# Performance work log

Measured on AMD Instinct MI355X. Metric: run time of the kernel, lower is better.

The kernel has to match this reference:

```python
import jax, jax.numpy as jnp
import numpy as np

LOG2 = float(np.log(2.0))

def ssp(x):
    # shifted softplus: softplus(x) - log(2)
    return jax.nn.softplus(x) - LOG2

N_NODES = 50000
N_EDGES = 600000
HID = 128
NF = 128

def setup_inputs() -> dict:
    key = jax.random.key(0)
    ks = jax.random.split(key, 10)
    x = jax.random.normal(ks[0], (N_NODES, HID), dtype=jnp.float32)
    edge_attr = jax.random.normal(ks[1], (N_EDGES, NF), dtype=jnp.float32)
    edge_index = jax.random.randint(ks[2], (2, N_EDGES), 0, N_NODES, dtype=jnp.int32)
    s = 1.0 / np.sqrt(NF)
    fc1_w = jax.random.uniform(ks[3], (NF, HID), jnp.float32, -s, s)   # CFConv.fc1 (no bias)
    f_w1 = jax.random.uniform(ks[4], (NF, NF), jnp.float32, -s, s)     # filter_mlp[0]
    f_b1 = jnp.zeros((NF,), jnp.float32)
    f_w2 = jax.random.uniform(ks[5], (NF, NF), jnp.float32, -s, s)     # filter_mlp[2]
    f_b2 = jnp.zeros((NF,), jnp.float32)
    s_w1 = jax.random.uniform(ks[6], (NF, NF), jnp.float32, -s, s)     # StateMLP.fc1
    s_w2 = jax.random.uniform(ks[7], (NF, NF), jnp.float32, -s, s)     # StateMLP.fc2
    return {"x": x, "edge_attr": edge_attr, "edge_index": edge_index,
            "fc1_w": fc1_w, "f_w1": f_w1, "f_b1": f_b1, "f_w2": f_w2,
            "f_b2": f_b2, "s_w1": s_w1, "s_w2": s_w2}

def reference(x, edge_attr, edge_index, fc1_w, f_w1, f_b1, f_w2, f_b2, s_w1, s_w2):
    src, dst = edge_index[0], edge_index[1]  # x_j = x[src], aggregate at dst
    # filter network on edge attributes: [E, NF]
    W = ssp(ssp(edge_attr @ f_w1.T + f_b1) @ f_w2.T + f_b2)
    # message: gather source nodes, linear transform, filter multiply
    msg = (x[src] @ fc1_w.T) * W                               # [E, NF]
    # scatter-add aggregation into nodes
    agg = jax.ops.segment_sum(msg, dst, num_segments=x.shape[0])  # [N, NF]
    # StateMLP
    return ssp(agg @ s_w1.T) @ s_w2.T
```

## Files before the change

kernel.cpp:

```cpp
#include <hip/hip_runtime.h>

#define F 128

typedef __attribute__((ext_vector_type(8))) __bf16 bf16x8;
typedef __attribute__((ext_vector_type(4))) float floatx4;

__device__ __forceinline__ float ssp(float x) {
    return __logf(fmaf(0.5f, __expf(x), 0.5f));
}

__global__ void prep_kernel(const float* __restrict__ fc1w,
                            const float* __restrict__ fw1,
                            const float* __restrict__ fw2,
                            const float* __restrict__ sw1,
                            const float* __restrict__ sw2,
                            __bf16* __restrict__ fc1h, __bf16* __restrict__ fc1l,
                            __bf16* __restrict__ fw1h, __bf16* __restrict__ fw2h,
                            __bf16* __restrict__ sw1h, __bf16* __restrict__ sw1l,
                            __bf16* __restrict__ sw2h, __bf16* __restrict__ sw2l)
{
    int i = blockIdx.x * blockDim.x + threadIdx.x;
    if (i >= F * F) return;
    float v; __bf16 h;
    v = fc1w[i]; h = (__bf16)v; fc1h[i] = h; fc1l[i] = (__bf16)(v - (float)h);
    v = sw1[i];  h = (__bf16)v; sw1h[i] = h; sw1l[i] = (__bf16)(v - (float)h);
    v = sw2[i];  h = (__bf16)v; sw2h[i] = h; sw2l[i] = (__bf16)(v - (float)h);
    fw1h[i] = (__bf16)fw1[i];
    fw2h[i] = (__bf16)fw2[i];
}

__global__ __launch_bounds__(256) void fc1_kernel(
    const float* __restrict__ x, const __bf16* __restrict__ wh,
    const __bf16* __restrict__ wl, float* __restrict__ y, int M)
{
    const int tid = threadIdx.x;
    const int wv = tid >> 6, lane = tid & 63;
    const int m16 = lane & 15, q = lane >> 4;
    const int g = wv & 1, c = wv >> 1;
    const int rowA0 = blockIdx.x * 32 + g * 16 + m16;
    const int rowA = rowA0 < M ? rowA0 : M - 1;

    floatx4 acc[4] = {};
    #pragma unroll
    for (int ks = 0; ks < 4; ++ks) {
        const int kb = ks * 32 + q * 8;
        const float4* p = (const float4*)(x + (size_t)rowA * F + kb);
        float4 a0 = p[0], a1 = p[1];
        float fv[8] = {a0.x, a0.y, a0.z, a0.w, a1.x, a1.y, a1.z, a1.w};
        bf16x8 ah, al;
        #pragma unroll
        for (int i = 0; i < 8; ++i) {
            __bf16 h = (__bf16)fv[i];
            ah[i] = h; al[i] = (__bf16)(fv[i] - (float)h);
        }
        #pragma unroll
        for (int nt = 0; nt < 4; ++nt) {
            const size_t wo = (size_t)(c * 64 + nt * 16 + m16) * F + kb;
            bf16x8 bh = *(const bf16x8*)(wh + wo);
            bf16x8 bl = *(const bf16x8*)(wl + wo);
            acc[nt] = __builtin_amdgcn_mfma_f32_16x16x32_bf16(ah, bh, acc[nt], 0, 0, 0);
            acc[nt] = __builtin_amdgcn_mfma_f32_16x16x32_bf16(al, bh, acc[nt], 0, 0, 0);
            acc[nt] = __builtin_amdgcn_mfma_f32_16x16x32_bf16(ah, bl, acc[nt], 0, 0, 0);
        }
    }
    const int rowD0 = blockIdx.x * 32 + g * 16 + q * 4;
    #pragma unroll
    for (int nt = 0; nt < 4; ++nt) {
        const int col = c * 64 + nt * 16 + m16;
        #pragma unroll
        for (int r = 0; r < 4; ++r) {
            const int row = rowD0 + r;
            if (row < M) y[(size_t)row * F + col] = acc[nt][r];
        }
    }
}

__global__ __launch_bounds__(256) void edge_kernel(
    const float* __restrict__ edge_attr,
    const int* __restrict__ eidx,
    const float* __restrict__ fb1, const float* __restrict__ fb2,
    const __bf16* __restrict__ fw1, const __bf16* __restrict__ fw2,
    const float* __restrict__ y,
    float* __restrict__ agg, int E)
{
    __shared__ __bf16 h1[64][136];

    const int tid = threadIdx.x;
    const int wv = tid >> 6, lane = tid & 63;
    const int m16 = lane & 15, q = lane >> 4;
    const int e0 = blockIdx.x * 64;
    const int rowA0 = e0 + wv * 16 + m16;
    const int rowA = rowA0 < E ? rowA0 : E - 1;

    floatx4 acc[8] = {};
    #pragma unroll
    for (int ks = 0; ks < 4; ++ks) {
        const int kb = ks * 32 + q * 8;
        const float4* pa = (const float4*)(edge_attr + (size_t)rowA * F + kb);
        float4 a0 = pa[0], a1 = pa[1];
        float fv[8] = {a0.x, a0.y, a0.z, a0.w, a1.x, a1.y, a1.z, a1.w};
        bf16x8 aF;
        #pragma unroll
        for (int i = 0; i < 8; ++i) aF[i] = (__bf16)fv[i];
        #pragma unroll
        for (int nt = 0; nt < 8; ++nt) {
            bf16x8 bF = *(const bf16x8*)(fw1 + (size_t)(nt * 16 + m16) * F + kb);
            acc[nt] = __builtin_amdgcn_mfma_f32_16x16x32_bf16(aF, bF, acc[nt], 0, 0, 0);
        }
    }
    #pragma unroll
    for (int nt = 0; nt < 8; ++nt) {
        const int col = nt * 16 + m16;
        const float b = fb1[col];
        #pragma unroll
        for (int r = 0; r < 4; ++r) {
            const int row = wv * 16 + q * 4 + r;
            h1[row][col] = (__bf16)ssp(acc[nt][r] + b);
        }
    }
    __syncthreads();

    floatx4 zero = {};
    #pragma unroll
    for (int nt = 0; nt < 8; ++nt) acc[nt] = zero;
    #pragma unroll
    for (int ks = 0; ks < 4; ++ks) {
        const int kb = ks * 32 + q * 8;
        bf16x8 aF = *(const bf16x8*)(&h1[wv * 16 + m16][kb]);
        #pragma unroll
        for (int nt = 0; nt < 8; ++nt) {
            bf16x8 bF = *(const bf16x8*)(fw2 + (size_t)(nt * 16 + m16) * F + kb);
            acc[nt] = __builtin_amdgcn_mfma_f32_16x16x32_bf16(aF, bF, acc[nt], 0, 0, 0);
        }
    }

    int src[4], dst[4], ok[4];
    #pragma unroll
    for (int r = 0; r < 4; ++r) {
        const int e = e0 + wv * 16 + q * 4 + r;
        const int ec = e < E ? e : E - 1;
        ok[r] = (e < E);
        src[r] = eidx[ec];
        dst[r] = eidx[E + ec];
    }
    #pragma unroll
    for (int nt = 0; nt < 8; ++nt) {
        const int col = nt * 16 + m16;
        const float b = fb2[col];
        #pragma unroll
        for (int r = 0; r < 4; ++r) {
            if (ok[r]) {
                const float wV = ssp(acc[nt][r] + b);
                const float v = y[(size_t)src[r] * F + col] * wV;
                unsafeAtomicAdd(&agg[(size_t)dst[r] * F + col], v);
            }
        }
    }
}

__global__ __launch_bounds__(256) void state_kernel(
    const float* __restrict__ agg,
    const __bf16* __restrict__ w1h, const __bf16* __restrict__ w1l,
    const __bf16* __restrict__ w2h, const __bf16* __restrict__ w2l,
    float* __restrict__ out, int M)
{
    __shared__ __bf16 hh[32][136];
    __shared__ __bf16 hl[32][136];

    const int tid = threadIdx.x;
    const int wv = tid >> 6, lane = tid & 63;
    const int m16 = lane & 15, q = lane >> 4;
    const int g = wv & 1, c = wv >> 1;
    const int rowA0 = blockIdx.x * 32 + g * 16 + m16;
    const int rowA = rowA0 < M ? rowA0 : M - 1;

    floatx4 acc[4] = {};
    #pragma unroll
    for (int ks = 0; ks < 4; ++ks) {
        const int kb = ks * 32 + q * 8;
        const float4* p = (const float4*)(agg + (size_t)rowA * F + kb);
        float4 a0 = p[0], a1 = p[1];
        float fv[8] = {a0.x, a0.y, a0.z, a0.w, a1.x, a1.y, a1.z, a1.w};
        bf16x8 ah, al;
        #pragma unroll
        for (int i = 0; i < 8; ++i) {
            __bf16 h = (__bf16)fv[i];
            ah[i] = h; al[i] = (__bf16)(fv[i] - (float)h);
        }
        #pragma unroll
        for (int nt = 0; nt < 4; ++nt) {
            const size_t wo = (size_t)(c * 64 + nt * 16 + m16) * F + kb;
            bf16x8 bh = *(const bf16x8*)(w1h + wo);
            bf16x8 bl = *(const bf16x8*)(w1l + wo);
            acc[nt] = __builtin_amdgcn_mfma_f32_16x16x32_bf16(ah, bh, acc[nt], 0, 0, 0);
            acc[nt] = __builtin_amdgcn_mfma_f32_16x16x32_bf16(al, bh, acc[nt], 0, 0, 0);
            acc[nt] = __builtin_amdgcn_mfma_f32_16x16x32_bf16(ah, bl, acc[nt], 0, 0, 0);
        }
    }
    #pragma unroll
    for (int nt = 0; nt < 4; ++nt) {
        const int col = c * 64 + nt * 16 + m16;
        #pragma unroll
        for (int r = 0; r < 4; ++r) {
            const int row = g * 16 + q * 4 + r;
            const float h = ssp(acc[nt][r]);
            const __bf16 H = (__bf16)h;
            hh[row][col] = H;
            hl[row][col] = (__bf16)(h - (float)H);
        }
    }
    __syncthreads();

    floatx4 zero = {};
    #pragma unroll
    for (int nt = 0; nt < 4; ++nt) acc[nt] = zero;
    #pragma unroll
    for (int ks = 0; ks < 4; ++ks) {
        const int kb = ks * 32 + q * 8;
        bf16x8 aH = *(const bf16x8*)(&hh[g * 16 + m16][kb]);
        bf16x8 aL = *(const bf16x8*)(&hl[g * 16 + m16][kb]);
        #pragma unroll
        for (int nt = 0; nt < 4; ++nt) {
            const size_t wo = (size_t)(c * 64 + nt * 16 + m16) * F + kb;
            bf16x8 bh = *(const bf16x8*)(w2h + wo);
            bf16x8 bl = *(const bf16x8*)(w2l + wo);
            acc[nt] = __builtin_amdgcn_mfma_f32_16x16x32_bf16(aH, bh, acc[nt], 0, 0, 0);
            acc[nt] = __builtin_amdgcn_mfma_f32_16x16x32_bf16(aL, bh, acc[nt], 0, 0, 0);
            acc[nt] = __builtin_amdgcn_mfma_f32_16x16x32_bf16(aH, bl, acc[nt], 0, 0, 0);
        }
    }
    const int rowD0 = blockIdx.x * 32 + g * 16 + q * 4;
    #pragma unroll
    for (int nt = 0; nt < 4; ++nt) {
        const int col = c * 64 + nt * 16 + m16;
        #pragma unroll
        for (int r = 0; r < 4; ++r) {
            const int row = rowD0 + r;
            if (row < M) out[(size_t)row * F + col] = acc[nt][r];
        }
    }
}

extern "C" void kernel_launch(void* const* d_in, const int* in_sizes, int n_in,
                              void* d_out, int out_size, void* d_ws, size_t ws_size,
                              hipStream_t stream)
{
    const float* x         = (const float*)d_in[0];
    const float* edge_attr = (const float*)d_in[1];
    const int*   eidx      = (const int*)d_in[2];
    const float* fc1w      = (const float*)d_in[3];
    const float* fw1       = (const float*)d_in[4];
    const float* fb1       = (const float*)d_in[5];
    const float* fw2       = (const float*)d_in[6];
    const float* fb2       = (const float*)d_in[7];
    const float* sw1       = (const float*)d_in[8];
    const float* sw2       = (const float*)d_in[9];
    float* out = (float*)d_out;

    const int N = in_sizes[0] / F;
    const int E = in_sizes[1] / F;

    float* agg = (float*)d_ws;
    float* y   = agg + (size_t)N * F;
    __bf16* wb = (__bf16*)(y + (size_t)N * F);
    const int WSZ = F * F;
    __bf16* fc1h = wb;            __bf16* fc1l = wb + WSZ;
    __bf16* fw1h = wb + 2 * WSZ;  __bf16* fw2h = wb + 3 * WSZ;
    __bf16* sw1h = wb + 4 * WSZ;  __bf16* sw1l = wb + 5 * WSZ;
    __bf16* sw2h = wb + 6 * WSZ;  __bf16* sw2l = wb + 7 * WSZ;

    hipMemsetAsync(agg, 0, (size_t)N * F * sizeof(float), stream);

    prep_kernel<<<(WSZ + 255) / 256, 256, 0, stream>>>(
        fc1w, fw1, fw2, sw1, sw2, fc1h, fc1l, fw1h, fw2h, sw1h, sw1l, sw2h, sw2l);

    fc1_kernel<<<(N + 31) / 32, 256, 0, stream>>>(x, fc1h, fc1l, y, N);

    edge_kernel<<<(E + 63) / 64, 256, 0, stream>>>(
        edge_attr, eidx, fb1, fb2, fw1h, fw2h, y, agg, E);

    state_kernel<<<(N + 31) / 32, 256, 0, stream>>>(
        agg, sw1h, sw1l, sw2h, sw2l, out, N);
}
```

Before: 931.1 us.

## Sort edges by destination and segment-reduce messages before atomic adds

Builds a counting-sort permutation of edges by destination node (histogram, single-block scan, scatter) and processes edges in that order. Messages are staged in shared memory and each thread reduces runs of equal destination along a column before issuing one atomic add per run. This is meant to cut global atomic traffic sharply, at the cost of extra sort kernels, gathered edge_attr reads and an extra barrier. The bounds guard for a partial last block is dropped.

```diff
diff --git a/kernel.cpp b/kernel.cpp
--- a/kernel.cpp
+++ b/kernel.cpp
@@ -29,6 +29,49 @@
     fw2h[i] = (__bf16)fw2[i];
 }
 
+__global__ void hist_kernel(const int* __restrict__ eidx, int* __restrict__ deg, int E)
+{
+    int e = blockIdx.x * blockDim.x + threadIdx.x;
+    if (e < E) atomicAdd(&deg[eidx[E + e]], 1);
+}
+
+__global__ __launch_bounds__(1024) void scan_kernel(int* __restrict__ cur, int N)
+{
+    __shared__ int part[1024];
+    const int t = threadIdx.x;
+    const int chunk = (N + 1023) / 1024;
+    const int lo = t * chunk;
+    const int hi = (lo + chunk < N) ? lo + chunk : N;
+    int s = 0;
+    for (int i = lo; i < hi; ++i) s += cur[i];
+    part[t] = s;
+    __syncthreads();
+    for (int off = 1; off < 1024; off <<= 1) {
+        int v = part[t];
+        int u = (t >= off) ? part[t - off] : 0;
+        __syncthreads();
+        part[t] = v + u;
+        __syncthreads();
+    }
+    int pre = (t == 0) ? 0 : part[t - 1];
+    for (int i = lo; i < hi; ++i) {
+        int d = cur[i];
+        cur[i] = pre;
+        pre += d;
+    }
+}
+
+__global__ void scatter_kernel(const int* __restrict__ eidx, int* __restrict__ cur,
+                               int* __restrict__ perm, int E)
+{
+    int e = blockIdx.x * blockDim.x + threadIdx.x;
+    if (e < E) {
+        int d = eidx[E + e];
+        int pos = atomicAdd(&cur[d], 1);
+        perm[pos] = e;
+    }
+}
+
 __global__ __launch_bounds__(256) void fc1_kernel(
     const float* __restrict__ x, const __bf16* __restrict__ wh,
     const __bf16* __restrict__ wl, float* __restrict__ y, int M)
@@ -78,25 +121,35 @@
 __global__ __launch_bounds__(256) void edge_kernel(
     const float* __restrict__ edge_attr,
     const int* __restrict__ eidx,
+    const int* __restrict__ perm,
     const float* __restrict__ fb1, const float* __restrict__ fb2,
     const __bf16* __restrict__ fw1, const __bf16* __restrict__ fw2,
     const float* __restrict__ y,
     float* __restrict__ agg, int E)
 {
-    __shared__ __bf16 h1[64][136];
+    __shared__ float msgF[64][132];
+    __shared__ int sOE[64], sSRC[64], sDST[64];
+    __bf16 (*h1)[136] = (__bf16 (*)[136])&msgF[0][0];
 
     const int tid = threadIdx.x;
     const int wv = tid >> 6, lane = tid & 63;
     const int m16 = lane & 15, q = lane >> 4;
     const int e0 = blockIdx.x * 64;
-    const int rowA0 = e0 + wv * 16 + m16;
-    const int rowA = rowA0 < E ? rowA0 : E - 1;
-
+
+    if (tid < 64) {
+        const int oe = perm[e0 + tid];
+        sOE[tid] = oe;
+        sSRC[tid] = eidx[oe];
+        sDST[tid] = eidx[E + oe];
+    }
+    __syncthreads();
+
+    const int aRow = sOE[wv * 16 + m16];
     floatx4 acc[8] = {};
     #pragma unroll
     for (int ks = 0; ks < 4; ++ks) {
         const int kb = ks * 32 + q * 8;
-        const float4* pa = (const float4*)(edge_attr + (size_t)rowA * F + kb);
+        const float4* pa = (const float4*)(edge_attr + (size_t)aRow * F + kb);
         float4 a0 = pa[0], a1 = pa[1];
         float fv[8] = {a0.x, a0.y, a0.z, a0.w, a1.x, a1.y, a1.z, a1.w};
         bf16x8 aF;
@@ -133,29 +186,41 @@
             acc[nt] = __builtin_amdgcn_mfma_f32_16x16x32_bf16(aF, bF, acc[nt], 0, 0, 0);
         }
     }
-
-    int src[4], dst[4], ok[4];
-    #pragma unroll
-    for (int r = 0; r < 4; ++r) {
-        const int e = e0 + wv * 16 + q * 4 + r;
-        const int ec = e < E ? e : E - 1;
-        ok[r] = (e < E);
-        src[r] = eidx[ec];
-        dst[r] = eidx[E + ec];
-    }
+    __syncthreads();
+
+    int srcR[4];
+    #pragma unroll
+    for (int r = 0; r < 4; ++r) srcR[r] = sSRC[wv * 16 + q * 4 + r];
     #pragma unroll
     for (int nt = 0; nt < 8; ++nt) {
         const int col = nt * 16 + m16;
         const float b = fb2[col];
         #pragma unroll
         for (int r = 0; r < 4; ++r) {
-            if (ok[r]) {
-                const float wV = ssp(acc[nt][r] + b);
-                const float v = y[(size_t)src[r] * F + col] * wV;
-                unsafeAtomicAdd(&agg[(size_t)dst[r] * F + col], v);
-            }
-        }
-    }
+            const int row = wv * 16 + q * 4 + r;
+            const float wV = ssp(acc[nt][r] + b);
+            msgF[row][col] = y[(size_t)srcR[r] * F + col] * wV;
+        }
+    }
+    __syncthreads();
+
+    const int col = tid & 127;
+    const int r0 = (tid >> 7) * 32;
+    float a = msgF[r0][col];
+    int cur = sDST[r0];
+    #pragma unroll 1
+    for (int i = 1; i < 32; ++i) {
+        const int row = r0 + i;
+        const int d = sDST[row];
+        const float v = msgF[row][col];
+        if (d != cur) {
+            unsafeAtomicAdd(&agg[(size_t)cur * F + col], a);
+            a = v; cur = d;
+        } else {
+            a += v;
+        }
+    }
+    unsafeAtomicAdd(&agg[(size_t)cur * F + col], a);
 }
 
 __global__ __launch_bounds__(256) void state_kernel(
@@ -262,7 +327,9 @@
 
     float* agg = (float*)d_ws;
     float* y   = agg + (size_t)N * F;
-    __bf16* wb = (__bf16*)(y + (size_t)N * F);
+    int*   cur = (int*)(y + (size_t)N * F);
+    int*   perm = cur + N;
+    __bf16* wb = (__bf16*)(perm + E);
     const int WSZ = F * F;
     __bf16* fc1h = wb;            __bf16* fc1l = wb + WSZ;
     __bf16* fw1h = wb + 2 * WSZ;  __bf16* fw2h = wb + 3 * WSZ;
@@ -270,14 +337,19 @@
     __bf16* sw2h = wb + 6 * WSZ;  __bf16* sw2l = wb + 7 * WSZ;
 
     hipMemsetAsync(agg, 0, (size_t)N * F * sizeof(float), stream);
+    hipMemsetAsync(cur, 0, (size_t)N * sizeof(int), stream);
 
     prep_kernel<<<(WSZ + 255) / 256, 256, 0, stream>>>(
         fc1w, fw1, fw2, sw1, sw2, fc1h, fc1l, fw1h, fw2h, sw1h, sw1l, sw2h, sw2l);
 
+    hist_kernel<<<(E + 255) / 256, 256, 0, stream>>>(eidx, cur, E);
+    scan_kernel<<<1, 1024, 0, stream>>>(cur, N);
+    scatter_kernel<<<(E + 255) / 256, 256, 0, stream>>>(eidx, cur, perm, E);
+
     fc1_kernel<<<(N + 31) / 32, 256, 0, stream>>>(x, fc1h, fc1l, y, N);
 
     edge_kernel<<<(E + 63) / 64, 256, 0, stream>>>(
-        edge_attr, eidx, fb1, fb2, fw1h, fw2h, y, agg, E);
+        edge_attr, eidx, perm, fb1, fb2, fw1h, fw2h, y, agg, E);
 
     state_kernel<<<(N + 31) / 32, 256, 0, stream>>>(
         agg, sw1h, sw1l, sw2h, sw2l, out, N);
```

Result: slower. 1.033 ms (+11.0%).
